# Optimization experiments

Hardware: AMD Instinct MI355X
Metric: run time of the kernel (lower is better)

Reference implementation:

```python
import jax, jax.numpy as jnp
import numpy as np

HASH_BUCKETS = 1024
D_MODEL = 256


def setup_inputs() -> dict:
    key = jax.random.key(0)
    ks = jax.random.split(key, 12)
    batch_a, batch_b, n_keys, d = 4096, 8192, 4, D_MODEL
    inp = {
        "table_a_emb": jax.random.normal(ks[0], (batch_a, d), dtype=jnp.float32),
        "table_b_emb": jax.random.normal(ks[1], (batch_b, d), dtype=jnp.float32),
        "keys_a": jax.random.randint(ks[2], (batch_a, n_keys), 0, 1000000, dtype=jnp.int64) if jax.config.jax_enable_x64 else jax.random.randint(ks[2], (batch_a, n_keys), 0, 1000000, dtype=jnp.int32),
        "keys_b": jax.random.randint(ks[3], (batch_b, n_keys), 0, 1000000, dtype=jnp.int64) if jax.config.jax_enable_x64 else jax.random.randint(ks[3], (batch_b, n_keys), 0, 1000000, dtype=jnp.int32),
        # SimpleMLP(d_in=2d, d_hidden=2d, n_hidden=1, d_out=d): in->hidden ReLU, hidden->out
        "W1": jax.random.normal(ks[4], (2 * d, 2 * d), dtype=jnp.float32) * (1.0 / np.sqrt(2 * d)),
        "b1": jnp.zeros((2 * d,), dtype=jnp.float32),
        "W2": jax.random.normal(ks[5], (2 * d, d), dtype=jnp.float32) * (1.0 / np.sqrt(2 * d)),
        "b2": jnp.zeros((d,), dtype=jnp.float32),
        "Wo": jax.random.normal(ks[6], (d, d), dtype=jnp.float32) * (1.0 / np.sqrt(d)),
        "bo": jnp.zeros((d,), dtype=jnp.float32),
    }
    return inp


def reference(table_a_emb, table_b_emb, keys_a, keys_b, W1, b1, W2, b2, Wo, bo):
    # hash-bucket matching: row i of table_a matches all rows of table_b with equal hash
    hash_a = jnp.sum(keys_a, axis=1) % HASH_BUCKETS  # (batch_a,)
    hash_b = jnp.sum(keys_b, axis=1) % HASH_BUCKETS  # (batch_b,)
    mask = (hash_a[:, None] == hash_b[None, :]).astype(table_b_emb.dtype)  # (batch_a, batch_b)
    count = mask.sum(axis=1, keepdims=True)  # (batch_a, 1)
    # mean of matched table_b embeddings; zeros when no match (matches torch loop semantics)
    agg_b = (mask @ table_b_emb) / jnp.maximum(count, 1.0)  # (batch_a, d)
    combined = jnp.concatenate([table_a_emb, agg_b], axis=-1)  # (batch_a, 2d)
    h = jax.nn.relu(combined @ W1 + b1)
    rel = h @ W2 + b2
    return rel @ Wo + bo
```

## Files before the change

### kernel.cpp

```cpp
#include <hip/hip_runtime.h>
#include <hip/hip_bf16.h>

#define HASH_BUCKETS 1024
#define BA 4096
#define BB 8192

typedef __attribute__((ext_vector_type(8))) short bf16x8;
typedef __attribute__((ext_vector_type(4))) float f32x4;

__device__ __forceinline__ short f2bf(float x) {
    union { float f; unsigned int u; } c;
    c.f = x;
    unsigned int lsb = (c.u >> 16) & 1u;
    c.u += 0x7fffu + lsb;
    return (short)(c.u >> 16);
}

__device__ __forceinline__ void gl_lds16(const void* g, void* l) {
    __builtin_amdgcn_global_load_lds((const __attribute__((address_space(1))) void*)g,
                                     (__attribute__((address_space(3))) void*)l, 16, 0, 0);
}

__global__ __launch_bounds__(256) void prep_kernel(
    const float* __restrict__ W1, const float* __restrict__ Wo,
    const float* __restrict__ W2, const float* __restrict__ b2,
    const float* __restrict__ bo, const float* __restrict__ ta,
    const float* __restrict__ tb, const int* __restrict__ ka,
    const int* __restrict__ kb, short* __restrict__ W1T,
    short* __restrict__ w2woT, short* __restrict__ tab,
    int* __restrict__ ha, float* __restrict__ bfused,
    short* __restrict__ bmean) {
    __shared__ __align__(16) char smem[36896];
    const int blk = blockIdx.x;
    const int t = threadIdx.x;
    if (blk < 64) {
        float(*tl)[65] = (float(*)[65])smem;
        const int tr = (blk >> 3) * 64, tc = (blk & 7) * 64;
        const int c = t & 63, r0 = t >> 6;
#pragma unroll
        for (int i = 0; i < 16; ++i) {
            int r = r0 + i * 4;
            tl[r][c] = W1[(size_t)(tr + r) * 512 + tc + c];
        }
        __syncthreads();
#pragma unroll
        for (int i = 0; i < 16; ++i) {
            int r = r0 + i * 4;
            W1T[(size_t)(tc + r) * 512 + tr + c] = f2bf(tl[c][r]);
        }
    } else if (blk < 96) {
        float* As = (float*)smem;
        float* Bs = (float*)(smem + 8704);
        const int b = blk - 64;
        const int bn = (b & 3) * 64;
        const int bm = (b >> 2) * 64;
        const int tx = t & 15, ty = t >> 4;
        float acc[4][4] = {};
        for (int c0 = 0; c0 < 256; c0 += 32) {
            {
                const int cc = t & 31, mb = t >> 5;
#pragma unroll
                for (int mi = 0; mi < 8; ++mi) {
                    int m = mi * 8 + mb;
                    As[cc * 68 + m] = W2[(size_t)(bm + m) * 256 + c0 + cc];
                }
            }
            {
                const int nn = t & 63, cb = t >> 6;
#pragma unroll
                for (int ci = 0; ci < 8; ++ci) {
                    int c = ci * 4 + cb;
                    Bs[c * 68 + nn] = Wo[(size_t)(c0 + c) * 256 + bn + nn];
                }
            }
            __syncthreads();
#pragma unroll
            for (int cc = 0; cc < 32; ++cc) {
                float4 a = *(const float4*)&As[cc * 68 + ty * 4];
                float4 bv = *(const float4*)&Bs[cc * 68 + tx * 4];
                acc[0][0] += a.x * bv.x; acc[0][1] += a.x * bv.y; acc[0][2] += a.x * bv.z; acc[0][3] += a.x * bv.w;
                acc[1][0] += a.y * bv.x; acc[1][1] += a.y * bv.y; acc[1][2] += a.y * bv.z; acc[1][3] += a.y * bv.w;
                acc[2][0] += a.z * bv.x; acc[2][1] += a.z * bv.y; acc[2][2] += a.z * bv.z; acc[2][3] += a.z * bv.w;
                acc[3][0] += a.w * bv.x; acc[3][1] += a.w * bv.y; acc[3][2] += a.w * bv.z; acc[3][3] += a.w * bv.w;
            }
            __syncthreads();
        }
#pragma unroll
        for (int r = 0; r < 4; ++r)
#pragma unroll
            for (int c = 0; c < 4; ++c) {
                int k = bm + ty * 4 + r, n = bn + tx * 4 + c;
                w2woT[(size_t)n * 512 + k] = f2bf(acc[r][c]);
            }
    } else if (blk < 160) {
        const int b = blk - 96;
#pragma unroll
        for (int i = 0; i < 16; ++i) {
            int e = b * 4096 + i * 256 + t;
            float4 v = ((const float4*)ta)[e];
            short4 s;
            s.x = f2bf(v.x); s.y = f2bf(v.y); s.z = f2bf(v.z); s.w = f2bf(v.w);
            ((short4*)tab)[e] = s;
        }
    } else if (blk < 176) {
        const int r = (blk - 160) * 256 + t;
        int4 k4 = ((const int4*)ka)[r];
        ha[r] = (k4.x + k4.y + k4.z + k4.w) & (HASH_BUCKETS - 1);
    } else if (blk == 176) {
        float acc = bo[t];
        for (int k = 0; k < 256; ++k) acc += b2[k] * Wo[(size_t)k * 256 + t];
        bfused[t] = acc;
    } else {
        int* sh = (int*)smem;
        float* part = (float*)(smem + 32768);
        int* pcnt = (int*)(smem + 36864);
        const int h = blk - 177;
        const int w = t >> 6, l = t & 63;
#pragma unroll 4
        for (int i = 0; i < 32; ++i) {
            int r = i * 256 + t;
            int4 k4 = ((const int4*)kb)[r];
            sh[r] = (k4.x + k4.y + k4.z + k4.w) & (HASH_BUCKETS - 1);
        }
        __syncthreads();
        float a0 = 0.f, a1 = 0.f, a2 = 0.f, a3 = 0.f;
        int cnt = 0;
#pragma unroll 4
        for (int it = 0; it < 32; ++it) {
            int base = w * 2048 + it * 64;
            unsigned long long m = __ballot(sh[base + l] == h);
            cnt += __popcll(m);
            while (m) {
                int j = base + (__ffsll((long long)m) - 1);
                m &= (m - 1);
                const float* row = tb + (size_t)j * 256;
                a0 += row[l];
                a1 += row[l + 64];
                a2 += row[l + 128];
                a3 += row[l + 192];
            }
        }
        part[w * 256 + l] = a0;
        part[w * 256 + l + 64] = a1;
        part[w * 256 + l + 128] = a2;
        part[w * 256 + l + 192] = a3;
        if (l == 0) pcnt[w] = cnt;
        __syncthreads();
        float s = part[t] + part[256 + t] + part[512 + t] + part[768 + t];
        int c = pcnt[0] + pcnt[1] + pcnt[2] + pcnt[3];
        bmean[(size_t)h * 256 + t] = f2bf(s / (float)max(c, 1));
    }
}

template <int MODE>
__global__ __launch_bounds__(256) void mfgemm(const short* __restrict__ A,
                                              const short* __restrict__ Bt,
                                              const short* __restrict__ tab,
                                              const short* __restrict__ bmean,
                                              const int* __restrict__ ha,
                                              const float* __restrict__ bias,
                                              void* __restrict__ Cv,
                                              int M, int N, int K) {
    __shared__ short As[64 * 32];
    __shared__ short Bs[64 * 32];
    const int tid = threadIdx.x;
    const int l = tid & 63, w = tid >> 6;
    const int wm = w >> 1, wn = w & 1;
    const int bm = blockIdx.y * 64, bn = blockIdx.x * 64;

    const int srow = l >> 2;
    const int skoff = (l & 3) * 8;
    const int arow = bm + w * 16 + srow;
    const int brow = bn + w * 16 + srow;
    int ha_r = 0;
    if (MODE == 0) ha_r = ha[arow];
    short* a_dst = &As[(w * 16) * 32];
    short* b_dst = &Bs[(w * 16) * 32];

    const int lr = l & 15, kf = (l >> 4) * 8;
    f32x4 acc[2][2] = {};

    for (int k0 = 0; k0 < K; k0 += 32) {
        const short* asrc;
        if (MODE == 0)
            asrc = (k0 < 256) ? &tab[(size_t)arow * 256 + k0 + skoff]
                              : &bmean[(size_t)ha_r * 256 + (k0 - 256) + skoff];
        else
            asrc = &A[(size_t)arow * K + k0 + skoff];
        gl_lds16(asrc, a_dst);
        gl_lds16(&Bt[(size_t)brow * K + k0 + skoff], b_dst);
        __syncthreads();
        bf16x8 af0 = *(const bf16x8*)&As[(wm * 32 + lr) * 32 + kf];
        bf16x8 af1 = *(const bf16x8*)&As[(wm * 32 + 16 + lr) * 32 + kf];
        bf16x8 bf0 = *(const bf16x8*)&Bs[(wn * 32 + lr) * 32 + kf];
        bf16x8 bf1 = *(const bf16x8*)&Bs[(wn * 32 + 16 + lr) * 32 + kf];
        acc[0][0] = __builtin_amdgcn_mfma_f32_16x16x32_bf16(af0, bf0, acc[0][0], 0, 0, 0);
        acc[0][1] = __builtin_amdgcn_mfma_f32_16x16x32_bf16(af0, bf1, acc[0][1], 0, 0, 0);
        acc[1][0] = __builtin_amdgcn_mfma_f32_16x16x32_bf16(af1, bf0, acc[1][0], 0, 0, 0);
        acc[1][1] = __builtin_amdgcn_mfma_f32_16x16x32_bf16(af1, bf1, acc[1][1], 0, 0, 0);
        __syncthreads();
    }

#pragma unroll
    for (int mf = 0; mf < 2; ++mf)
#pragma unroll
        for (int nf = 0; nf < 2; ++nf) {
            const int col = bn + wn * 32 + nf * 16 + lr;
            const int rbase = bm + wm * 32 + mf * 16 + ((l >> 4) << 2);
            const float bv = bias[col];
#pragma unroll
            for (int i = 0; i < 4; ++i) {
                const float x = acc[mf][nf][i] + bv;
                const int row = rbase + i;
                if (MODE == 0)
                    ((short*)Cv)[(size_t)row * N + col] = f2bf(fmaxf(x, 0.f));
                else
                    ((float*)Cv)[(size_t)row * N + col] = x;
            }
        }
}

extern "C" void kernel_launch(void* const* d_in, const int* in_sizes, int n_in,
                              void* d_out, int out_size, void* d_ws, size_t ws_size,
                              hipStream_t stream) {
    const float* ta = (const float*)d_in[0];
    const float* tb = (const float*)d_in[1];
    const int* ka = (const int*)d_in[2];
    const int* kb = (const int*)d_in[3];
    const float* W1 = (const float*)d_in[4];
    const float* b1 = (const float*)d_in[5];
    const float* W2 = (const float*)d_in[6];
    const float* b2 = (const float*)d_in[7];
    const float* Wo = (const float*)d_in[8];
    const float* bo = (const float*)d_in[9];
    float* out = (float*)d_out;

    char* ws = (char*)d_ws;
    int* ha = (int*)(ws + 0);
    short* bmean = (short*)(ws + 16384);
    short* tab = (short*)(ws + 540672);
    short* W1T = (short*)(ws + 2637824);
    short* w2woT = (short*)(ws + 3162112);
    float* bfused = (float*)(ws + 3424256);
    short* hbuf = (short*)(ws + 3425280);

    prep_kernel<<<1201, 256, 0, stream>>>(W1, Wo, W2, b2, bo, ta, tb, ka, kb,
                                          W1T, w2woT, tab, ha, bfused, bmean);
    mfgemm<0><<<dim3(8, 64), 256, 0, stream>>>(nullptr, W1T, tab, bmean, ha, b1,
                                               hbuf, BA, 512, 512);
    mfgemm<1><<<dim3(4, 64), 256, 0, stream>>>(hbuf, w2woT, nullptr, nullptr, nullptr,
                                               bfused, out, BA, 256, 512);
}
```

Baseline: 37.58 us.

## Double-buffer LDS tiles with K=64 steps and XOR-swizzled layout in mfgemm

Restructures the MFMA GEMM main loop to use two LDS buffers so the next K tile is loaded via global_load_lds while the current tile is computed. It also doubles the K step to 64, which halves the number of barriers per tile, and XOR-swizzles the LDS column layout to reduce bank conflicts on the fragment reads. In exchange, LDS use quadruples and the kernel relies on an explicit vmcnt wait, which adds some occupancy and correctness risk.

Result: faster. 35.44 us (-5.7%).

```diff
diff --git a/kernel.cpp b/kernel.cpp
--- a/kernel.cpp
+++ b/kernel.cpp
@@ -161,43 +161,86 @@
                                               const float* __restrict__ bias,
                                               void* __restrict__ Cv,
                                               int M, int N, int K) {
-    __shared__ short As[64 * 32];
-    __shared__ short Bs[64 * 32];
+    __shared__ short As[2][64 * 64];
+    __shared__ short Bs[2][64 * 64];
     const int tid = threadIdx.x;
     const int l = tid & 63, w = tid >> 6;
     const int wm = w >> 1, wn = w & 1;
     const int bm = blockIdx.y * 64, bn = blockIdx.x * 64;
 
-    const int srow = l >> 2;
-    const int skoff = (l & 3) * 8;
-    const int arow = bm + w * 16 + srow;
-    const int brow = bn + w * 16 + srow;
-    int ha_r = 0;
-    if (MODE == 0) ha_r = ha[arow];
-    short* a_dst = &As[(w * 16) * 32];
-    short* b_dst = &Bs[(w * 16) * 32];
-
-    const int lr = l & 15, kf = (l >> 4) * 8;
+    const int r0 = (w * 2 + 0) * 8 + (l >> 3);
+    const int r1 = (w * 2 + 1) * 8 + (l >> 3);
+    const int sk0 = ((l & 7) ^ (r0 & 7)) * 8;
+    const int sk1 = ((l & 7) ^ (r1 & 7)) * 8;
+    const int arow0 = bm + r0, arow1 = bm + r1;
+    const int brow0 = bn + r0, brow1 = bn + r1;
+    int ha0 = 0, ha1 = 0;
+    if (MODE == 0) { ha0 = ha[arow0]; ha1 = ha[arow1]; }
+    const int dst0 = (w * 2 + 0) * 512;
+    const int dst1 = (w * 2 + 1) * 512;
+
+    const int lr = l & 15;
+    const int g = l >> 4;
     f32x4 acc[2][2] = {};
 
-    for (int k0 = 0; k0 < K; k0 += 32) {
-        const short* asrc;
-        if (MODE == 0)
-            asrc = (k0 < 256) ? &tab[(size_t)arow * 256 + k0 + skoff]
-                              : &bmean[(size_t)ha_r * 256 + (k0 - 256) + skoff];
-        else
-            asrc = &A[(size_t)arow * K + k0 + skoff];
-        gl_lds16(asrc, a_dst);
-        gl_lds16(&Bt[(size_t)brow * K + k0 + skoff], b_dst);
-        __syncthreads();
-        bf16x8 af0 = *(const bf16x8*)&As[(wm * 32 + lr) * 32 + kf];
-        bf16x8 af1 = *(const bf16x8*)&As[(wm * 32 + 16 + lr) * 32 + kf];
-        bf16x8 bf0 = *(const bf16x8*)&Bs[(wn * 32 + lr) * 32 + kf];
-        bf16x8 bf1 = *(const bf16x8*)&Bs[(wn * 32 + 16 + lr) * 32 + kf];
-        acc[0][0] = __builtin_amdgcn_mfma_f32_16x16x32_bf16(af0, bf0, acc[0][0], 0, 0, 0);
-        acc[0][1] = __builtin_amdgcn_mfma_f32_16x16x32_bf16(af0, bf1, acc[0][1], 0, 0, 0);
-        acc[1][0] = __builtin_amdgcn_mfma_f32_16x16x32_bf16(af1, bf0, acc[1][0], 0, 0, 0);
-        acc[1][1] = __builtin_amdgcn_mfma_f32_16x16x32_bf16(af1, bf1, acc[1][1], 0, 0, 0);
+    auto STAGE = [&](int nb, int kt) {
+        const int k0 = kt * 64;
+        const short *as0, *as1;
+        if (MODE == 0) {
+            if (k0 < 256) {
+                as0 = &tab[(size_t)arow0 * 256 + k0 + sk0];
+                as1 = &tab[(size_t)arow1 * 256 + k0 + sk1];
+            } else {
+                as0 = &bmean[(size_t)ha0 * 256 + (k0 - 256) + sk0];
+                as1 = &bmean[(size_t)ha1 * 256 + (k0 - 256) + sk1];
+            }
+        } else {
+            as0 = &A[(size_t)arow0 * K + k0 + sk0];
+            as1 = &A[(size_t)arow1 * K + k0 + sk1];
+        }
+        gl_lds16(as0, &As[nb][dst0]);
+        gl_lds16(as1, &As[nb][dst1]);
+        gl_lds16(&Bt[(size_t)brow0 * K + k0 + sk0], &Bs[nb][dst0]);
+        gl_lds16(&Bt[(size_t)brow1 * K + k0 + sk1], &Bs[nb][dst1]);
+    };
+
+    auto COMPUTE = [&](int nb) {
+        const short* ab = &As[nb][0];
+        const short* bb = &Bs[nb][0];
+        bf16x8 af[2][2], bfr[2][2];
+#pragma unroll
+        for (int mf = 0; mf < 2; ++mf) {
+            const int rr = wm * 32 + mf * 16 + lr;
+#pragma unroll
+            for (int ks = 0; ks < 2; ++ks)
+                af[mf][ks] = *(const bf16x8*)&ab[rr * 64 + (((ks * 4 + g) ^ (lr & 7)) * 8)];
+        }
+#pragma unroll
+        for (int nf = 0; nf < 2; ++nf) {
+            const int rr = wn * 32 + nf * 16 + lr;
+#pragma unroll
+            for (int ks = 0; ks < 2; ++ks)
+                bfr[nf][ks] = *(const bf16x8*)&bb[rr * 64 + (((ks * 4 + g) ^ (lr & 7)) * 8)];
+        }
+#pragma unroll
+        for (int ks = 0; ks < 2; ++ks)
+#pragma unroll
+            for (int mf = 0; mf < 2; ++mf)
+#pragma unroll
+                for (int nf = 0; nf < 2; ++nf)
+                    acc[mf][nf] = __builtin_amdgcn_mfma_f32_16x16x32_bf16(
+                        af[mf][ks], bfr[nf][ks], acc[mf][nf], 0, 0, 0);
+    };
+
+    const int nt = K >> 6;
+    STAGE(0, 0);
+    asm volatile("s_waitcnt vmcnt(0)" ::: "memory");
+    __syncthreads();
+    for (int t = 0; t < nt; ++t) {
+        const int cur = t & 1;
+        if (t + 1 < nt) STAGE(cur ^ 1, t + 1);
+        COMPUTE(cur);
+        asm volatile("s_waitcnt vmcnt(0)" ::: "memory");
         __syncthreads();
     }
 
```
